# Performance work log

Measured on AMD Instinct MI355X. Metric: run time of the kernel, lower is better.

## Reference

```python
import jax, jax.numpy as jnp
import numpy as np

B, N, D = 16, 1024, 768
H = 12
HS = D // H
L = 2  # n_ffn_layers
EPS = 1e-6


def layernorm(x, scale, bias):
    mu = jnp.mean(x, axis=-1, keepdims=True)
    var = jnp.var(x, axis=-1, keepdims=True)
    return (x - mu) * jax.lax.rsqrt(var + EPS) * scale + bias


def log_cosh(x):
    # numerically stable log(cosh(x)) = |x| + log1p(exp(-2|x|)) - log(2)
    ax = jnp.abs(x)
    return ax + jnp.log1p(jnp.exp(-2.0 * ax)) - jnp.log(2.0)


def setup_inputs() -> dict:
    key = jax.random.key(0)
    ks = jax.random.split(key, 8)
    x = jax.random.normal(ks[0], (B, N, D), dtype=jnp.float32)
    # pre-attention LayerNorm params
    ln1_scale = jnp.ones((D,), jnp.float32)
    ln1_bias = jnp.zeros((D,), jnp.float32)
    # per-head value projections [H, D, HS] (Dense, no bias)
    Wv = jax.random.normal(ks[1], (H, D, HS), jnp.float32) / np.sqrt(D)
    # per-head circulant rows alpha_delta [H, N], truncated_normal(stddev=sqrt(1/N))
    alpha = jax.random.truncated_normal(ks[2], -2.0, 2.0, (H, N), jnp.float32) * np.sqrt(1.0 / N)
    # FFN: L layers of Dense(D) + LayerNorm + swish
    Wf = jax.random.normal(ks[3], (L, D, D), jnp.float32) / np.sqrt(D)
    bf = jnp.zeros((L, D), jnp.float32)
    lnf_scale = jnp.ones((L, D), jnp.float32)
    lnf_bias = jnp.zeros((L, D), jnp.float32)
    return {"x": x, "ln1_scale": ln1_scale, "ln1_bias": ln1_bias, "Wv": Wv,
            "alpha": alpha, "Wf": Wf, "bf": bf,
            "lnf_scale": lnf_scale, "lnf_bias": lnf_bias}


def reference(x, ln1_scale, ln1_bias, Wv, alpha, Wf, bf, lnf_scale, lnf_bias):
    b, n, d = x.shape
    h, hs = Wv.shape[0], Wv.shape[2]
    # --- multi-head positional (circulant) attention on LN(x) ---
    xn = layernorm(x, ln1_scale, ln1_bias)
    v = jnp.einsum('bnd,hdk->bhnk', xn, Wv)  # per-head values
    # circulant matrix C[h, i, j] = alpha[h, (i - j) mod n]  (scipy.linalg.circulant)
    idx = (jnp.arange(n)[:, None] - jnp.arange(n)[None, :]) % n  # [n, n]
    C = alpha[:, idx]                                            # [h, n, n]
    y = jnp.einsum('hij,bhjk->bhik', C, v)                       # [b, h, n, hs]
    y = jnp.transpose(y, (0, 2, 1, 3)).reshape(b, n, h * hs)     # concat heads
    x = x + y
    # --- FFN: [Dense(D) -> LayerNorm -> swish] x L ---
    z = x
    for l in range(Wf.shape[0]):
        z = jax.nn.swish(layernorm(z @ Wf[l] + bf[l], lnf_scale[l], lnf_bias[l]))
    return log_cosh(z + x)
```

## Files before the change

kernel.cpp:

```cpp
#include <hip/hip_runtime.h>
#include <cstdint>
#include <cstddef>


typedef __attribute__((ext_vector_type(8))) short bf16x8;
typedef __attribute__((ext_vector_type(4))) float f32x4;
typedef __attribute__((ext_vector_type(4))) unsigned short us4;

__device__ __forceinline__ unsigned short f2bf(float f) {
  unsigned int u = __builtin_bit_cast(unsigned int, f);
  u += 0x7FFFu + ((u >> 16) & 1u);
  return (unsigned short)(u >> 16);
}
__device__ __forceinline__ float bf2f(unsigned short u) {
  return __builtin_bit_cast(float, (unsigned int)u << 16);
}

__device__ __forceinline__ void g2l16(const void* g, void* l) {
  __builtin_amdgcn_global_load_lds(
      (const __attribute__((address_space(1))) unsigned int*)g,
      (__attribute__((address_space(3))) unsigned int*)l,
      16, 0, 0);
}

#define WAITB(n) asm volatile("s_waitcnt vmcnt(" #n ") lgkmcnt(0)\n\ts_barrier" ::: "memory")

__global__ __launch_bounds__(256) void pack_w2t(const float* __restrict__ Wv,
                                                unsigned short* __restrict__ W2t) {
  int o = blockIdx.x * 256 + threadIdx.x;
  int np = o / 768, d = o - np * 768;
  int h = np >> 6, k = np & 63;
  W2t[o] = f2bf(Wv[h * 49152 + d * 64 + k]);
}

__global__ __launch_bounds__(256) void pack_wft(const float* __restrict__ Wf,
                                                unsigned short* __restrict__ Wft) {
  int o = blockIdx.x * 256 + threadIdx.x;
  int l = o / 589824, rem = o - l * 589824;
  int np = rem / 768, d = rem - np * 768;
  Wft[o] = f2bf(Wf[l * 589824 + d * 768 + np]);
}

__device__ __forceinline__ void wave_reduce2(float& s, float& s2) {
#pragma unroll
  for (int off = 32; off > 0; off >>= 1) {
    s += __shfl_down(s, off);
    s2 += __shfl_down(s2, off);
  }
  s = __shfl(s, 0);
  s2 = __shfl(s2, 0);
}

__global__ __launch_bounds__(256) void ln1_kernel(const float* __restrict__ x,
                                                  const float* __restrict__ sc,
                                                  const float* __restrict__ bi,
                                                  unsigned short* __restrict__ out) {
  int row = blockIdx.x * 4 + (threadIdx.x >> 6);
  int lane = threadIdx.x & 63;
  size_t base = (size_t)row * 768;
  float4 v[3];
#pragma unroll
  for (int j = 0; j < 3; ++j) v[j] = *(const float4*)(x + base + lane * 4 + j * 256);
  float s = 0.f, s2 = 0.f;
#pragma unroll
  for (int j = 0; j < 3; ++j) {
    s += v[j].x + v[j].y + v[j].z + v[j].w;
    s2 += v[j].x * v[j].x + v[j].y * v[j].y + v[j].z * v[j].z + v[j].w * v[j].w;
  }
  wave_reduce2(s, s2);
  float mu = s * (1.0f / 768.0f);
  float var = s2 * (1.0f / 768.0f) - mu * mu;
  float r = rsqrtf(var + 1e-6f);
#pragma unroll
  for (int j = 0; j < 3; ++j) {
    int d = lane * 4 + j * 256;
    float4 scv = *(const float4*)(sc + d);
    float4 biv = *(const float4*)(bi + d);
    us4 o;
    o[0] = f2bf((v[j].x - mu) * r * scv.x + biv.x);
    o[1] = f2bf((v[j].y - mu) * r * scv.y + biv.y);
    o[2] = f2bf((v[j].z - mu) * r * scv.z + biv.z);
    o[3] = f2bf((v[j].w - mu) * r * scv.w + biv.w);
    *(us4*)(out + base + d) = o;
  }
}

__global__ __launch_bounds__(256) void lnswish_kernel(const unsigned short* __restrict__ g,
                                                      const float* __restrict__ sc,
                                                      const float* __restrict__ bi,
                                                      unsigned short* __restrict__ out) {
  int row = blockIdx.x * 4 + (threadIdx.x >> 6);
  int lane = threadIdx.x & 63;
  size_t base = (size_t)row * 768;
  float v[3][4];
#pragma unroll
  for (int j = 0; j < 3; ++j) {
    us4 gv = *(const us4*)(g + base + lane * 4 + j * 256);
#pragma unroll
    for (int q = 0; q < 4; ++q) v[j][q] = bf2f(gv[q]);
  }
  float s = 0.f, s2 = 0.f;
#pragma unroll
  for (int j = 0; j < 3; ++j)
#pragma unroll
    for (int q = 0; q < 4; ++q) { s += v[j][q]; s2 += v[j][q] * v[j][q]; }
  wave_reduce2(s, s2);
  float mu = s * (1.0f / 768.0f);
  float var = s2 * (1.0f / 768.0f) - mu * mu;
  float r = rsqrtf(var + 1e-6f);
#pragma unroll
  for (int j = 0; j < 3; ++j) {
    int d = lane * 4 + j * 256;
    float4 scv = *(const float4*)(sc + d);
    float4 biv = *(const float4*)(bi + d);
    const float* scp = &scv.x;
    const float* bip = &biv.x;
    us4 o;
#pragma unroll
    for (int q = 0; q < 4; ++q) {
      float z = (v[j][q] - mu) * r * scp[q] + bip[q];
      o[q] = f2bf(z / (1.0f + __expf(-z)));
    }
    *(us4*)(out + base + d) = o;
  }
}

__global__ __launch_bounds__(256) void final_kernel(const unsigned short* __restrict__ g,
                                                    const float* __restrict__ sc,
                                                    const float* __restrict__ bi,
                                                    const unsigned short* __restrict__ x2,
                                                    float* __restrict__ out) {
  int row = blockIdx.x * 4 + (threadIdx.x >> 6);
  int lane = threadIdx.x & 63;
  size_t base = (size_t)row * 768;
  float v[3][4];
#pragma unroll
  for (int j = 0; j < 3; ++j) {
    us4 gv = *(const us4*)(g + base + lane * 4 + j * 256);
#pragma unroll
    for (int q = 0; q < 4; ++q) v[j][q] = bf2f(gv[q]);
  }
  float s = 0.f, s2 = 0.f;
#pragma unroll
  for (int j = 0; j < 3; ++j)
#pragma unroll
    for (int q = 0; q < 4; ++q) { s += v[j][q]; s2 += v[j][q] * v[j][q]; }
  wave_reduce2(s, s2);
  float mu = s * (1.0f / 768.0f);
  float var = s2 * (1.0f / 768.0f) - mu * mu;
  float r = rsqrtf(var + 1e-6f);
#pragma unroll
  for (int j = 0; j < 3; ++j) {
    int d = lane * 4 + j * 256;
    float4 scv = *(const float4*)(sc + d);
    float4 biv = *(const float4*)(bi + d);
    us4 xv = *(const us4*)(x2 + base + d);
    const float* scp = &scv.x;
    const float* bip = &biv.x;
    float4 o;
    float* op = &o.x;
#pragma unroll
    for (int q = 0; q < 4; ++q) {
      float z = (v[j][q] - mu) * r * scp[q] + bip[q];
      float sw = z / (1.0f + __expf(-z));
      float t = sw + bf2f(xv[q]);
      float ax = fabsf(t);
      op[q] = ax + __logf(1.0f + __expf(-2.0f * ax)) - 0.69314718055994531f;
    }
    *(float4*)(out + base + d) = o;
  }
}

__device__ __forceinline__ void gemm_core(const unsigned short* __restrict__ A,
                                          const unsigned short* __restrict__ Bt,
                                          int K, int m0, int n0,
                                          unsigned short* sA, unsigned short* sB,
                                          f32x4 acc[4][4]) {
  const int tid = threadIdx.x;
  const int wave = tid >> 6, lane = tid & 63;
  const int wm = (wave >> 1) << 6, wn = (wave & 1) << 6;
  const int fm = lane & 15, fq = lane >> 4;
  const int r0 = tid >> 2, r1 = r0 + 64;
  const int cg = tid & 3;
  const int cs0 = (cg ^ ((r0 >> 1) & 3)) << 3;
  const int cs1 = (cg ^ ((r1 >> 1) & 3)) << 3;
  const int ld0 = r0 * 32 + (cg << 3);
  const int ld1 = r1 * 32 + (cg << 3);
  const int niter = K >> 5;

#define STAGE(k0v, buf)                                                       \
  {                                                                           \
    unsigned short* dA = sA + (buf) * 4096;                                   \
    unsigned short* dB = sB + (buf) * 4096;                                   \
    g2l16(A + (size_t)(m0 + r0) * K + (k0v) + cs0, dA + ld0);                 \
    g2l16(Bt + (size_t)(n0 + r0) * K + (k0v) + cs0, dB + ld0);                \
    g2l16(A + (size_t)(m0 + r1) * K + (k0v) + cs1, dA + ld1);                 \
    g2l16(Bt + (size_t)(n0 + r1) * K + (k0v) + cs1, dB + ld1);                \
  }
#define GCOMP(bc)                                                             \
  {                                                                           \
    const unsigned short* pA = sA + (bc) * 4096;                              \
    const unsigned short* pB = sB + (bc) * 4096;                              \
    bf16x8 aq[4], bq[4];                                                      \
    _Pragma("unroll") for (int t = 0; t < 4; ++t) {                           \
      int ra = wm + (t << 4) + fm;                                            \
      int rb = wn + (t << 4) + fm;                                            \
      aq[t] = *(const bf16x8*)(pA + (ra << 5) + ((fq ^ ((ra >> 1) & 3)) << 3)); \
      bq[t] = *(const bf16x8*)(pB + (rb << 5) + ((fq ^ ((rb >> 1) & 3)) << 3)); \
    }                                                                         \
    _Pragma("unroll") for (int mt = 0; mt < 4; ++mt)                          \
    _Pragma("unroll") for (int nt = 0; nt < 4; ++nt)                          \
      acc[mt][nt] = __builtin_amdgcn_mfma_f32_16x16x32_bf16(aq[mt], bq[nt],   \
                                                            acc[mt][nt], 0, 0, 0); \
  }

  STAGE(0, 0);
  STAGE(32, 1);
  int bs = 2, bc = 0;
  for (int it = 0; it < niter - 1; ++it) {
    WAITB(4);
    if (it + 2 < niter) {
      STAGE((it + 2) << 5, bs);
      bs = (bs == 2) ? 0 : bs + 1;
    }
    GCOMP(bc);
    bc = (bc == 2) ? 0 : bc + 1;
  }
  WAITB(0);
  GCOMP(bc);
#undef STAGE
}

__device__ __forceinline__ void decode_mn_768(int f, int& m0, int& n0) {
  int xcd = f & 7, s = f >> 3;
  int g = s / 6, bx = s - g * 6;
  m0 = (xcd + g * 8) << 7;
  n0 = bx << 7;
}

__global__ __launch_bounds__(256, 3) void gemm1_kernel(const unsigned short* __restrict__ A,
                                                       const unsigned short* __restrict__ Bt,
                                                       unsigned short* __restrict__ Vt) {
  __shared__ unsigned short sA[3 * 4096];
  __shared__ unsigned short sB[3 * 4096];
  f32x4 acc[4][4] = {};
  int m0, n0;
  decode_mn_768(blockIdx.x, m0, n0);
  gemm_core(A, Bt, 768, m0, n0, sA, sB, acc);
  const int wave = threadIdx.x >> 6, lane = threadIdx.x & 63;
  const int wm = (wave >> 1) << 6, wn = (wave & 1) << 6;
  const int fm = lane & 15, fq = lane >> 4;
#pragma unroll
  for (int mt = 0; mt < 4; ++mt) {
    int rowb = m0 + wm + (mt << 4) + (fq << 2);
    int b = rowb >> 10, n = rowb & 1023;
#pragma unroll
    for (int nt = 0; nt < 4; ++nt) {
      int col = n0 + wn + (nt << 4) + fm;
      int h = col >> 6, ck = col & 63;
      size_t off = ((size_t)h << 20) + (size_t)((b << 6) + ck) * 1024 + n;
      us4 v;
#pragma unroll
      for (int r = 0; r < 4; ++r) v[r] = f2bf(acc[mt][nt][r]);
      *(us4*)(Vt + off) = v;
    }
  }
}

__global__ __launch_bounds__(256, 3) void circ_kernel(const float* __restrict__ alpha,
                                                      const unsigned short* __restrict__ Vt,
                                                      const float* __restrict__ xin,
                                                      unsigned short* __restrict__ x2bf) {
  __shared__ unsigned short sAc[8 * 1168];
  __shared__ unsigned short sB[4 * 4096];
  f32x4 acc[4][4] = {};
  int f = blockIdx.x;
  int xcd = f & 7, s = f >> 3;
  int h = s >> 3, t = s & 7;
  int mr = xcd >> 1, nr = xcd & 1;
  int m0 = ((mr << 1) + (t >> 2)) << 7;
  int n0 = ((nr << 2) + (t & 3)) << 7;

  const int tid = threadIdx.x;
  const int wave = tid >> 6, lane = tid & 63;
  const int wm = (wave >> 1) << 6, wn = (wave & 1) << 6;
  const int fm = lane & 15, fq = lane >> 4;

  const float* ah = alpha + (h << 10);
#pragma unroll
  for (int c = 0; c < 8; ++c)
    for (int u = tid; u < 1160; u += 256)
      sAc[c * 1168 + u] = f2bf(ah[(m0 - 897 - u - c) & 1023]);
  asm volatile("s_waitcnt vmcnt(0)" ::: "memory");

  const unsigned short* Bt = Vt + ((size_t)h << 20);
  const int r0 = tid >> 2, r1 = r0 + 64;
  const int cg = tid & 3;
  const int cs0 = (cg ^ ((r0 >> 1) & 3)) << 3;
  const int cs1 = (cg ^ ((r1 >> 1) & 3)) << 3;
  const int ld0 = r0 * 32 + (cg << 3);
  const int ld1 = r1 * 32 + (cg << 3);

#define STAGEB(k0v, buf)                                                      \
  {                                                                           \
    unsigned short* dB = sB + (buf) * 4096;                                   \
    g2l16(Bt + (size_t)(n0 + r0) * 1024 + (k0v) + cs0, dB + ld0);             \
    g2l16(Bt + (size_t)(n0 + r1) * 1024 + (k0v) + cs1, dB + ld1);             \
  }
#define CCOMP(it)                                                             \
  {                                                                           \
    const unsigned short* pB = sB + ((it) & 3) * 4096;                        \
    int k0v = (it) << 5;                                                      \
    bf16x8 aq[4], bq[4];                                                      \
    _Pragma("unroll") for (int t_ = 0; t_ < 4; ++t_) {                        \
      int rl = wm + (t_ << 4) + fm;                                           \
      int d = k0v + (fq << 3) + 127 - rl;                                     \
      int c = d & 7;                                                          \
      aq[t_] = *(const bf16x8*)(sAc + c * 1168 + (d - c));                    \
      int rb = wn + (t_ << 4) + fm;                                           \
      bq[t_] = *(const bf16x8*)(pB + (rb << 5) + ((fq ^ ((rb >> 1) & 3)) << 3)); \
    }                                                                         \
    _Pragma("unroll") for (int mt = 0; mt < 4; ++mt)                          \
    _Pragma("unroll") for (int nt = 0; nt < 4; ++nt)                          \
      acc[mt][nt] = __builtin_amdgcn_mfma_f32_16x16x32_bf16(aq[mt], bq[nt],   \
                                                            acc[mt][nt], 0, 0, 0); \
  }

  STAGEB(0, 0);
  STAGEB(32, 1);
  STAGEB(64, 2);
  for (int it = 0; it < 30; ++it) {
    WAITB(4);
    if (it < 29) STAGEB((it + 3) << 5, (it + 3) & 3);
    CCOMP(it);
  }
  WAITB(2);
  CCOMP(30);
  WAITB(0);
  CCOMP(31);
#undef STAGEB

#pragma unroll
  for (int mt = 0; mt < 4; ++mt) {
    int ib = m0 + wm + (mt << 4) + (fq << 2);
#pragma unroll
    for (int nt = 0; nt < 4; ++nt) {
      int c = n0 + wn + (nt << 4) + fm;
      int b = c >> 6, k = c & 63;
      size_t off = ((size_t)(b << 10) + ib) * 768 + (h << 6) + k;
#pragma unroll
      for (int r = 0; r < 4; ++r) {
        float val = acc[mt][nt][r] + xin[off + (size_t)r * 768];
        x2bf[off + (size_t)r * 768] = f2bf(val);
      }
    }
  }
}

__global__ __launch_bounds__(256, 3) void gemmf_kernel(const unsigned short* __restrict__ A,
                                                       const unsigned short* __restrict__ Bt,
                                                       const float* __restrict__ bias,
                                                       unsigned short* __restrict__ g) {
  __shared__ unsigned short sA[3 * 4096];
  __shared__ unsigned short sB[3 * 4096];
  f32x4 acc[4][4] = {};
  int m0, n0;
  decode_mn_768(blockIdx.x, m0, n0);
  gemm_core(A, Bt, 768, m0, n0, sA, sB, acc);
  const int wave = threadIdx.x >> 6, lane = threadIdx.x & 63;
  const int wm = (wave >> 1) << 6, wn = (wave & 1) << 6;
  const int fm = lane & 15, fq = lane >> 4;
#pragma unroll
  for (int mt = 0; mt < 4; ++mt) {
    int rowb = m0 + wm + (mt << 4) + (fq << 2);
#pragma unroll
    for (int nt = 0; nt < 4; ++nt) {
      int col = n0 + wn + (nt << 4) + fm;
      float bc = bias[col];
#pragma unroll
      for (int r = 0; r < 4; ++r)
        g[(size_t)(rowb + r) * 768 + col] = f2bf(acc[mt][nt][r] + bc);
    }
  }
}

extern "C" void kernel_launch(void* const* d_in, const int* in_sizes, int n_in,
                              void* d_out, int out_size, void* d_ws, size_t ws_size,
                              hipStream_t stream) {
  const float* x = (const float*)d_in[0];
  const float* ln1_s = (const float*)d_in[1];
  const float* ln1_b = (const float*)d_in[2];
  const float* Wv = (const float*)d_in[3];
  const float* alpha = (const float*)d_in[4];
  const float* Wf = (const float*)d_in[5];
  const float* bf = (const float*)d_in[6];
  const float* lnf_s = (const float*)d_in[7];
  const float* lnf_b = (const float*)d_in[8];
  float* out = (float*)d_out;

  char* ws = (char*)d_ws;
  unsigned short* slotA = (unsigned short*)ws;
  unsigned short* Vt = (unsigned short*)(ws + 25165824);
  unsigned short* gbf = Vt;
  unsigned short* slotX = (unsigned short*)(ws + 50331648);
  unsigned short* W2t = (unsigned short*)(ws + 75497472);
  unsigned short* Wft = (unsigned short*)(ws + 76677120);

  pack_w2t<<<2304, 256, 0, stream>>>(Wv, W2t);
  pack_wft<<<4608, 256, 0, stream>>>(Wf, Wft);

  ln1_kernel<<<4096, 256, 0, stream>>>(x, ln1_s, ln1_b, slotA);
  gemm1_kernel<<<768, 256, 0, stream>>>(slotA, W2t, Vt);
  circ_kernel<<<768, 256, 0, stream>>>(alpha, Vt, x, slotX);
  gemmf_kernel<<<768, 256, 0, stream>>>(slotX, Wft, bf, gbf);
  lnswish_kernel<<<4096, 256, 0, stream>>>(gbf, lnf_s, lnf_b, slotA);
  gemmf_kernel<<<768, 256, 0, stream>>>(slotA, Wft + 589824, bf + 768, gbf);
  final_kernel<<<4096, 256, 0, stream>>>(gbf, lnf_s + 768, lnf_b + 768, slotX, out);
}
```

Baseline: 278.0 us.

## Deepen A-operand prefetch in GEMMs and widen circulant B pipeline to five stages

The shared GEMM core now stages A tiles four deep and weight (B) tiles only two deep, issuing B one iteration ahead and A three ahead under separate waits. In the circulant kernel, the shifted-alpha LDS copies drop from eight to four, and A fragments are assembled from two 4-element loads. The freed LDS goes to a five-buffer B pipeline with four tiles in flight. The aim is to hide more global-load latency without raising LDS use, at the cost of two 8-byte LDS reads per A fragment and more complex wait counting.

New measurement: 284.8 us. +2.4%, slower.

```diff
diff --git a/kernel.cpp b/kernel.cpp
--- a/kernel.cpp
+++ b/kernel.cpp
@@ -4,6 +4,7 @@
 
 
 typedef __attribute__((ext_vector_type(8))) short bf16x8;
+typedef __attribute__((ext_vector_type(4))) short bf16x4;
 typedef __attribute__((ext_vector_type(4))) float f32x4;
 typedef __attribute__((ext_vector_type(4))) unsigned short us4;
 
@@ -188,19 +189,22 @@
   const int ld1 = r1 * 32 + (cg << 3);
   const int niter = K >> 5;
 
-#define STAGE(k0v, buf)                                                       \
+#define STAGEA(k0v, buf)                                                      \
   {                                                                           \
     unsigned short* dA = sA + (buf) * 4096;                                   \
+    g2l16(A + (size_t)(m0 + r0) * K + (k0v) + cs0, dA + ld0);                 \
+    g2l16(A + (size_t)(m0 + r1) * K + (k0v) + cs1, dA + ld1);                 \
+  }
+#define STAGEBW(k0v, buf)                                                     \
+  {                                                                           \
     unsigned short* dB = sB + (buf) * 4096;                                   \
-    g2l16(A + (size_t)(m0 + r0) * K + (k0v) + cs0, dA + ld0);                 \
     g2l16(Bt + (size_t)(n0 + r0) * K + (k0v) + cs0, dB + ld0);                \
-    g2l16(A + (size_t)(m0 + r1) * K + (k0v) + cs1, dA + ld1);                 \
     g2l16(Bt + (size_t)(n0 + r1) * K + (k0v) + cs1, dB + ld1);                \
   }
-#define GCOMP(bc)                                                             \
+#define GCOMP(it)                                                             \
   {                                                                           \
-    const unsigned short* pA = sA + (bc) * 4096;                              \
-    const unsigned short* pB = sB + (bc) * 4096;                              \
+    const unsigned short* pA = sA + ((it) & 3) * 4096;                        \
+    const unsigned short* pB = sB + ((it) & 1) * 4096;                        \
     bf16x8 aq[4], bq[4];                                                      \
     _Pragma("unroll") for (int t = 0; t < 4; ++t) {                           \
       int ra = wm + (t << 4) + fm;                                            \
@@ -214,21 +218,18 @@
                                                             acc[mt][nt], 0, 0, 0); \
   }
 
-  STAGE(0, 0);
-  STAGE(32, 1);
-  int bs = 2, bc = 0;
-  for (int it = 0; it < niter - 1; ++it) {
-    WAITB(4);
-    if (it + 2 < niter) {
-      STAGE((it + 2) << 5, bs);
-      bs = (bs == 2) ? 0 : bs + 1;
-    }
-    GCOMP(bc);
-    bc = (bc == 2) ? 0 : bc + 1;
-  }
-  WAITB(0);
-  GCOMP(bc);
-#undef STAGE
+  STAGEA(0, 0);
+  STAGEA(32, 1);
+  STAGEBW(0, 0);
+  STAGEA(64, 2);
+  for (int it = 0; it < niter; ++it) {
+    if (it < niter - 2) { WAITB(2); } else { WAITB(0); }
+    if (it + 1 < niter) STAGEBW((it + 1) << 5, (it + 1) & 1);
+    if (it + 3 < niter) STAGEA((it + 3) << 5, (it + 3) & 3);
+    GCOMP(it);
+  }
+#undef STAGEA
+#undef STAGEBW
 }
 
 __device__ __forceinline__ void decode_mn_768(int f, int& m0, int& n0) {
@@ -241,8 +242,8 @@
 __global__ __launch_bounds__(256, 3) void gemm1_kernel(const unsigned short* __restrict__ A,
                                                        const unsigned short* __restrict__ Bt,
                                                        unsigned short* __restrict__ Vt) {
-  __shared__ unsigned short sA[3 * 4096];
-  __shared__ unsigned short sB[3 * 4096];
+  __shared__ unsigned short sA[4 * 4096];
+  __shared__ unsigned short sB[2 * 4096];
   f32x4 acc[4][4] = {};
   int m0, n0;
   decode_mn_768(blockIdx.x, m0, n0);
@@ -271,8 +272,8 @@
                                                       const unsigned short* __restrict__ Vt,
                                                       const float* __restrict__ xin,
                                                       unsigned short* __restrict__ x2bf) {
-  __shared__ unsigned short sAc[8 * 1168];
-  __shared__ unsigned short sB[4 * 4096];
+  __shared__ unsigned short sAc[4 * 1168];
+  __shared__ unsigned short sB[5 * 4096];
   f32x4 acc[4][4] = {};
   int f = blockIdx.x;
   int xcd = f & 7, s = f >> 3;
@@ -288,7 +289,7 @@
 
   const float* ah = alpha + (h << 10);
 #pragma unroll
-  for (int c = 0; c < 8; ++c)
+  for (int c = 0; c < 4; ++c)
     for (int u = tid; u < 1160; u += 256)
       sAc[c * 1168 + u] = f2bf(ah[(m0 - 897 - u - c) & 1023]);
   asm volatile("s_waitcnt vmcnt(0)" ::: "memory");
@@ -307,16 +308,19 @@
     g2l16(Bt + (size_t)(n0 + r0) * 1024 + (k0v) + cs0, dB + ld0);             \
     g2l16(Bt + (size_t)(n0 + r1) * 1024 + (k0v) + cs1, dB + ld1);             \
   }
-#define CCOMP(it)                                                             \
+#define CCOMP(it, bsl)                                                        \
   {                                                                           \
-    const unsigned short* pB = sB + ((it) & 3) * 4096;                        \
+    const unsigned short* pB = sB + (bsl) * 4096;                             \
     int k0v = (it) << 5;                                                      \
     bf16x8 aq[4], bq[4];                                                      \
     _Pragma("unroll") for (int t_ = 0; t_ < 4; ++t_) {                        \
       int rl = wm + (t_ << 4) + fm;                                           \
       int d = k0v + (fq << 3) + 127 - rl;                                     \
-      int c = d & 7;                                                          \
-      aq[t_] = *(const bf16x8*)(sAc + c * 1168 + (d - c));                    \
+      int c2 = d & 3;                                                         \
+      const unsigned short* ap = sAc + c2 * 1168 + (d - c2);                  \
+      bf16x4 lo = *(const bf16x4*)ap;                                         \
+      bf16x4 hi = *(const bf16x4*)(ap + 4);                                   \
+      aq[t_] = __builtin_shufflevector(lo, hi, 0, 1, 2, 3, 4, 5, 6, 7);       \
       int rb = wn + (t_ << 4) + fm;                                           \
       bq[t_] = *(const bf16x8*)(pB + (rb << 5) + ((fq ^ ((rb >> 1) & 3)) << 3)); \
     }                                                                         \
@@ -329,15 +333,20 @@
   STAGEB(0, 0);
   STAGEB(32, 1);
   STAGEB(64, 2);
-  for (int it = 0; it < 30; ++it) {
-    WAITB(4);
-    if (it < 29) STAGEB((it + 3) << 5, (it + 3) & 3);
-    CCOMP(it);
-  }
-  WAITB(2);
-  CCOMP(30);
-  WAITB(0);
-  CCOMP(31);
+  STAGEB(96, 3);
+  int bs = 4, bc = 0;
+  for (int it = 0; it < 32; ++it) {
+    if (it <= 28) { WAITB(6); }
+    else if (it == 29) { WAITB(4); }
+    else if (it == 30) { WAITB(2); }
+    else { WAITB(0); }
+    if (it + 4 < 32) {
+      STAGEB((it + 4) << 5, bs);
+      bs = (bs == 4) ? 0 : bs + 1;
+    }
+    CCOMP(it, bc);
+    bc = (bc == 4) ? 0 : bc + 1;
+  }
 #undef STAGEB
 
 #pragma unroll
@@ -361,8 +370,8 @@
                                                        const unsigned short* __restrict__ Bt,
                                                        const float* __restrict__ bias,
                                                        unsigned short* __restrict__ g) {
-  __shared__ unsigned short sA[3 * 4096];
-  __shared__ unsigned short sB[3 * 4096];
+  __shared__ unsigned short sA[4 * 4096];
+  __shared__ unsigned short sB[2 * 4096];
   f32x4 acc[4][4] = {};
   int m0, n0;
   decode_mn_768(blockIdx.x, m0, n0);
```
